# Optimization experiments

Hardware: AMD Instinct MI355X
Metric: run time of the kernel (lower is better)

Reference implementation:

```python
import jax, jax.numpy as jnp
import numpy as np

N_SAMPLES = 16_777_216  # total surviving samples across all rays
N_RAY = 65_536          # number of rays


def setup_inputs() -> dict:
    key = jax.random.key(0)
    k1, k2 = jax.random.split(key)
    alpha = jax.random.uniform(k1, (N_SAMPLES,), dtype=jnp.float32)
    # sorted ray ids -> contiguous segments, as produced by create_full_step_id + masking
    ray_id = jnp.sort(jax.random.randint(k2, (N_SAMPLES,), 0, N_RAY, dtype=jnp.int32))
    return {"alpha": alpha, "ray_id": ray_id, "N_ray": N_RAY}


def _seg_prod_op(a, b):
    # segmented-product combine: reset the running product at segment starts
    va, fa = a
    vb, fb = b
    return jnp.where(fb, vb, va * vb), fa | fb


def reference(alpha, ray_id, N_ray):
    n = alpha.shape[0]
    one_minus_alpha = 1.0 - alpha + 1e-11                      # [n]
    is_start = jnp.concatenate(
        [jnp.ones((1,), jnp.bool_), ray_id[1:] != ray_id[:-1]]
    )                                                          # [n] segment starts
    # parallel segmented cumulative product (replaces the per-sample Python loop)
    cumprod, _ = jax.lax.associative_scan(_seg_prod_op, (one_minus_alpha, is_start))
    # NOTE: faithful to the source: transmittance is a global shift of cumprod
    # (cat([1, cumprod[:-1]])), NOT reset to 1 at each ray start.
    transmittance = jnp.concatenate([jnp.ones((1,), alpha.dtype), cumprod[:-1]])
    weights = alpha * transmittance                            # [n]
    # last sample index of each ray (ids are sorted, so max index == last write)
    last_idx = jnp.zeros((N_ray,), jnp.int32).at[ray_id].max(
        jnp.arange(n, dtype=jnp.int32)
    )                                                          # [N_ray]
    alphainv_last = cumprod[last_idx]                          # [N_ray]
    return weights, alphainv_last
```

## Files before the change

### kernel.cpp

```cpp
#include <hip/hip_runtime.h>
#include <stdint.h>


#define BLOCK 256
#define PT 32
#define NV (PT / 4)
#define CHUNK (BLOCK * PT)
#define NWAVE (BLOCK / 64)

struct Pair { float v; int f; };

__device__ __forceinline__ Pair seg_combine(Pair a, Pair b) {
    Pair r;
    r.v = b.f ? b.v : (a.v * b.v);
    r.f = a.f | b.f;
    return r;
}

__global__ __launch_bounds__(BLOCK, 4)
void nerf_reduce(const float* __restrict__ alpha, const int* __restrict__ ray_id,
                 float2* __restrict__ agg, float* __restrict__ alphainv,
                 int N_ray, int n) {
    const int c = blockIdx.x, t = threadIdx.x;
    const long gstart = (long)c * CHUNK + (long)t * PT;

    {
        int gid = c * BLOCK + t;
        if (gid < N_ray) alphainv[gid] = (1.0f - alpha[0]) + 1e-11f;
    }

    Pair run; run.v = 1.0f; run.f = 0;

    if (gstart + PT <= (long)n) {
        float4 AV[NV]; int4 RV[NV];
        #pragma unroll
        for (int q = 0; q < NV; ++q) {
            AV[q] = *(const float4*)(alpha  + gstart + 4 * q);
            RV[q] = *(const int4*)  (ray_id + gstart + 4 * q);
        }
        int prev = (gstart > 0) ? ray_id[gstart - 1] : -1;

        #pragma unroll
        for (int q = 0; q < NV; ++q) {
            const float4 av = AV[q]; const int4 rv = RV[q];
            Pair e;
            e.v = (1.0f - av.x) + 1e-11f; e.f = (rv.x != prev); run = seg_combine(run, e);
            e.v = (1.0f - av.y) + 1e-11f; e.f = (rv.y != rv.x); run = seg_combine(run, e);
            e.v = (1.0f - av.z) + 1e-11f; e.f = (rv.z != rv.y); run = seg_combine(run, e);
            e.v = (1.0f - av.w) + 1e-11f; e.f = (rv.w != rv.z); run = seg_combine(run, e);
            prev = rv.w;
        }
    } else if (gstart < (long)n) {
        int prev = (gstart > 0) ? ray_id[gstart - 1] : -1;
        for (int k = 0; k < PT; ++k) {
            long g = gstart + k;
            if (g < n) {
                int r = ray_id[g];
                Pair e; e.v = (1.0f - alpha[g]) + 1e-11f; e.f = (r != prev);
                prev = r;
                run = seg_combine(run, e);
            }
        }
    }

    #pragma unroll
    for (int off = 1; off < 64; off <<= 1) {
        Pair o;
        o.v = __shfl_down(run.v, off);
        o.f = __shfl_down(run.f, off);
        run = seg_combine(run, o);
    }

    __shared__ float s_wv[NWAVE];
    __shared__ int   s_wf[NWAVE];
    const int lane = t & 63, w = t >> 6;
    if (lane == 0) { s_wv[w] = run.v; s_wf[w] = run.f; }
    __syncthreads();
    if (t == 0) {
        Pair acc; acc.v = s_wv[0]; acc.f = s_wf[0];
        #pragma unroll
        for (int ww = 1; ww < NWAVE; ++ww) {
            Pair e; e.v = s_wv[ww]; e.f = s_wf[ww];
            acc = seg_combine(acc, e);
        }
        agg[c] = make_float2(acc.v, __int_as_float(acc.f));
    }
}

__global__ void nerf_init_rest(const float* __restrict__ alpha,
                               float* __restrict__ alphainv_tail, int count) {
    int i = blockIdx.x * blockDim.x + threadIdx.x;
    if (i < count) alphainv_tail[i] = (1.0f - alpha[0]) + 1e-11f;
}

__global__ __launch_bounds__(BLOCK, 3)
void nerf_apply(const float* __restrict__ alpha, const int* __restrict__ ray_id,
                const float2* __restrict__ agg,
                float* __restrict__ weights, float* __restrict__ alphainv, int n) {
    __shared__ float s_wv[NWAVE];
    __shared__ int   s_wf[NWAVE];
    __shared__ float s_pv;
    __shared__ int   s_pf;

    const int c = blockIdx.x, t = threadIdx.x;
    const int lane = t & 63, w = t >> 6;
    const long gstart = (long)c * CHUNK + (long)t * PT;

    if (t == 0) {
        Pair pre; pre.v = 1.0f; pre.f = 0;
        for (int j = c - 1; j >= 0; --j) {
            float2 g = agg[j];
            Pair e; e.v = g.x; e.f = __float_as_int(g.y);
            pre = (j == c - 1) ? e : seg_combine(e, pre);
            if (pre.f) break;
        }
        s_pv = pre.v; s_pf = pre.f;
    }

    const bool full = (gstart + PT) <= (long)n;
    float4 AV[NV]; int4 RV[NV];
    if (full) {
        #pragma unroll
        for (int q = 0; q < NV; ++q) {
            AV[q] = *(const float4*)(alpha  + gstart + 4 * q);
            RV[q] = *(const int4*)  (ray_id + gstart + 4 * q);
        }
    } else {
        #pragma unroll
        for (int q = 0; q < NV; ++q) {
            float aa[4]; int rr[4];
            #pragma unroll
            for (int k = 0; k < 4; ++k) {
                long g = gstart + 4 * q + k;
                aa[k] = (g < n) ? alpha[g]  : 0.0f;
                rr[k] = (g < n) ? ray_id[g] : -2;
            }
            AV[q] = make_float4(aa[0], aa[1], aa[2], aa[3]);
            RV[q] = make_int4(rr[0], rr[1], rr[2], rr[3]);
        }
    }
    const int prev0 = (gstart > 0 && gstart < (long)n) ? ray_id[gstart - 1] : -1;

    Pair loc; loc.v = 1.0f; loc.f = 0;
    {
        int prev = prev0;
        #pragma unroll
        for (int q = 0; q < NV; ++q) {
            const float4 av = AV[q]; const int4 rv = RV[q];
            if (full) {
                Pair e;
                e.v = (1.0f - av.x) + 1e-11f; e.f = (rv.x != prev); loc = seg_combine(loc, e);
                e.v = (1.0f - av.y) + 1e-11f; e.f = (rv.y != rv.x); loc = seg_combine(loc, e);
                e.v = (1.0f - av.z) + 1e-11f; e.f = (rv.z != rv.y); loc = seg_combine(loc, e);
                e.v = (1.0f - av.w) + 1e-11f; e.f = (rv.w != rv.z); loc = seg_combine(loc, e);
                prev = rv.w;
            } else {
                const float aa[4] = {av.x, av.y, av.z, av.w};
                const int   rr[4] = {rv.x, rv.y, rv.z, rv.w};
                #pragma unroll
                for (int k = 0; k < 4; ++k) {
                    long g = gstart + 4 * q + k;
                    if (g < n) {
                        Pair e; e.v = (1.0f - aa[k]) + 1e-11f; e.f = (rr[k] != prev);
                        prev = rr[k];
                        loc = seg_combine(loc, e);
                    }
                }
            }
        }
    }

    Pair inc = loc;
    #pragma unroll
    for (int off = 1; off < 64; off <<= 1) {
        Pair o;
        o.v = __shfl_up(inc.v, off);
        o.f = __shfl_up(inc.f, off);
        if (lane >= off) inc = seg_combine(o, inc);
    }
    Pair lexcl;
    {
        float uv = __shfl_up(inc.v, 1);
        int   uf = __shfl_up(inc.f, 1);
        if (lane == 0) { lexcl.v = 1.0f; lexcl.f = 0; }
        else           { lexcl.v = uv;   lexcl.f = uf; }
    }
    if (lane == 63) { s_wv[w] = inc.v; s_wf[w] = inc.f; }
    __syncthreads();

    Pair base; base.v = s_pv; base.f = s_pf;
    #pragma unroll
    for (int ww = 0; ww < NWAVE; ++ww) {
        if (ww < w) {
            Pair e; e.v = s_wv[ww]; e.f = s_wf[ww];
            base = seg_combine(base, e);
        }
    }
    Pair P = seg_combine(base, lexcl);

    {
        int prevRid = prev0;
        #pragma unroll
        for (int q = 0; q < NV; ++q) {
            const float4 av = AV[q]; const int4 rv = RV[q];
            const long e0 = gstart + 4 * q;
            if (full) {
                float w0, w1, w2, w3;
                int f = (rv.x != prevRid);
                w0 = av.x * P.v;
                if (f && e0 > 0) alphainv[prevRid] = P.v;
                { Pair e; e.v = (1.0f - av.x) + 1e-11f; e.f = f; P = seg_combine(P, e); }
                if (e0 == (long)n - 1) alphainv[rv.x] = P.v;
                f = (rv.y != rv.x);
                w1 = av.y * P.v;
                if (f) alphainv[rv.x] = P.v;
                { Pair e; e.v = (1.0f - av.y) + 1e-11f; e.f = f; P = seg_combine(P, e); }
                if (e0 + 1 == (long)n - 1) alphainv[rv.y] = P.v;
                f = (rv.z != rv.y);
                w2 = av.z * P.v;
                if (f) alphainv[rv.y] = P.v;
                { Pair e; e.v = (1.0f - av.z) + 1e-11f; e.f = f; P = seg_combine(P, e); }
                if (e0 + 2 == (long)n - 1) alphainv[rv.z] = P.v;
                f = (rv.w != rv.z);
                w3 = av.w * P.v;
                if (f) alphainv[rv.z] = P.v;
                { Pair e; e.v = (1.0f - av.w) + 1e-11f; e.f = f; P = seg_combine(P, e); }
                if (e0 + 3 == (long)n - 1) alphainv[rv.w] = P.v;

                *(float4*)(weights + e0) = make_float4(w0, w1, w2, w3);
            } else {
                const float aa[4] = {av.x, av.y, av.z, av.w};
                const int   rr[4] = {rv.x, rv.y, rv.z, rv.w};
                #pragma unroll
                for (int k = 0; k < 4; ++k) {
                    long g = e0 + k;
                    if (g < n) {
                        int f = (rr[k] != prevRid);
                        float wv = aa[k] * P.v;
                        if (f && g > 0) alphainv[prevRid] = P.v;
                        { Pair e; e.v = (1.0f - aa[k]) + 1e-11f; e.f = f; P = seg_combine(P, e); }
                        if (g == (long)n - 1) alphainv[rr[k]] = P.v;
                        weights[g] = wv;
                        prevRid = rr[k];
                    }
                }
            }
            if (full) prevRid = rv.w;
        }
    }
}

extern "C" void kernel_launch(void* const* d_in, const int* in_sizes, int n_in,
                              void* d_out, int out_size, void* d_ws, size_t ws_size,
                              hipStream_t stream) {
    const float* alpha  = (const float*)d_in[0];
    const int*   ray_id = (const int*)d_in[1];
    const int n     = in_sizes[0];
    const int N_ray = out_size - n;

    float* weights  = (float*)d_out;
    float* alphainv = weights + n;
    float2* agg     = (float2*)d_ws;

    const int nchunks = (n + CHUNK - 1) / CHUNK;

    nerf_reduce<<<nchunks, BLOCK, 0, stream>>>(alpha, ray_id, agg, alphainv, N_ray, n);
    if (N_ray > nchunks * BLOCK) {
        int extra = N_ray - nchunks * BLOCK;
        nerf_init_rest<<<(extra + BLOCK - 1) / BLOCK, BLOCK, 0, stream>>>(
            alpha, alphainv + nchunks * BLOCK, extra);
    }
    nerf_apply<<<nchunks, BLOCK, 0, stream>>>(alpha, ray_id, agg, weights, alphainv, n);
}
```

Baseline: 211.0 us.

## Fuse reduce and apply passes using per-block decoupled lookback over input windows

Replaces the two-pass reduce-then-apply segmented scan with a single kernel. Each block recomputes its incoming prefix by scanning preceding 1024-element windows of the input until a segment start is found. This removes one full read of alpha and ray_id and the workspace aggregate array, at the cost of redundant window reads and extra block-level syncs per block. Weight output now uses nontemporal stores, and launch bounds are relaxed, which may reduce occupancy.

```diff
diff --git a/kernel.cpp b/kernel.cpp
--- a/kernel.cpp
+++ b/kernel.cpp
@@ -7,6 +7,9 @@
 #define NV (PT / 4)
 #define CHUNK (BLOCK * PT)
 #define NWAVE (BLOCK / 64)
+#define LOOKW 1024
+
+typedef float nat_f4 __attribute__((ext_vector_type(4)));
 
 struct Pair { float v; int f; };
 
@@ -17,105 +20,25 @@
     return r;
 }
 
-__global__ __launch_bounds__(BLOCK, 4)
-void nerf_reduce(const float* __restrict__ alpha, const int* __restrict__ ray_id,
-                 float2* __restrict__ agg, float* __restrict__ alphainv,
-                 int N_ray, int n) {
-    const int c = blockIdx.x, t = threadIdx.x;
-    const long gstart = (long)c * CHUNK + (long)t * PT;
-
-    {
-        int gid = c * BLOCK + t;
-        if (gid < N_ray) alphainv[gid] = (1.0f - alpha[0]) + 1e-11f;
-    }
-
-    Pair run; run.v = 1.0f; run.f = 0;
-
-    if (gstart + PT <= (long)n) {
-        float4 AV[NV]; int4 RV[NV];
-        #pragma unroll
-        for (int q = 0; q < NV; ++q) {
-            AV[q] = *(const float4*)(alpha  + gstart + 4 * q);
-            RV[q] = *(const int4*)  (ray_id + gstart + 4 * q);
-        }
-        int prev = (gstart > 0) ? ray_id[gstart - 1] : -1;
-
-        #pragma unroll
-        for (int q = 0; q < NV; ++q) {
-            const float4 av = AV[q]; const int4 rv = RV[q];
-            Pair e;
-            e.v = (1.0f - av.x) + 1e-11f; e.f = (rv.x != prev); run = seg_combine(run, e);
-            e.v = (1.0f - av.y) + 1e-11f; e.f = (rv.y != rv.x); run = seg_combine(run, e);
-            e.v = (1.0f - av.z) + 1e-11f; e.f = (rv.z != rv.y); run = seg_combine(run, e);
-            e.v = (1.0f - av.w) + 1e-11f; e.f = (rv.w != rv.z); run = seg_combine(run, e);
-            prev = rv.w;
-        }
-    } else if (gstart < (long)n) {
-        int prev = (gstart > 0) ? ray_id[gstart - 1] : -1;
-        for (int k = 0; k < PT; ++k) {
-            long g = gstart + k;
-            if (g < n) {
-                int r = ray_id[g];
-                Pair e; e.v = (1.0f - alpha[g]) + 1e-11f; e.f = (r != prev);
-                prev = r;
-                run = seg_combine(run, e);
-            }
-        }
-    }
-
-    #pragma unroll
-    for (int off = 1; off < 64; off <<= 1) {
-        Pair o;
-        o.v = __shfl_down(run.v, off);
-        o.f = __shfl_down(run.f, off);
-        run = seg_combine(run, o);
-    }
-
-    __shared__ float s_wv[NWAVE];
-    __shared__ int   s_wf[NWAVE];
-    const int lane = t & 63, w = t >> 6;
-    if (lane == 0) { s_wv[w] = run.v; s_wf[w] = run.f; }
-    __syncthreads();
-    if (t == 0) {
-        Pair acc; acc.v = s_wv[0]; acc.f = s_wf[0];
-        #pragma unroll
-        for (int ww = 1; ww < NWAVE; ++ww) {
-            Pair e; e.v = s_wv[ww]; e.f = s_wf[ww];
-            acc = seg_combine(acc, e);
-        }
-        agg[c] = make_float2(acc.v, __int_as_float(acc.f));
-    }
-}
-
-__global__ void nerf_init_rest(const float* __restrict__ alpha,
-                               float* __restrict__ alphainv_tail, int count) {
+__global__ void nerf_init(const float* __restrict__ alpha,
+                          float* __restrict__ alphainv, int N_ray) {
     int i = blockIdx.x * blockDim.x + threadIdx.x;
-    if (i < count) alphainv_tail[i] = (1.0f - alpha[0]) + 1e-11f;
-}
-
-__global__ __launch_bounds__(BLOCK, 3)
-void nerf_apply(const float* __restrict__ alpha, const int* __restrict__ ray_id,
-                const float2* __restrict__ agg,
+    if (i < N_ray) alphainv[i] = (1.0f - alpha[0]) + 1e-11f;
+}
+
+__global__ __launch_bounds__(BLOCK, 2)
+void nerf_fused(const float* __restrict__ alpha, const int* __restrict__ ray_id,
                 float* __restrict__ weights, float* __restrict__ alphainv, int n) {
     __shared__ float s_wv[NWAVE];
     __shared__ int   s_wf[NWAVE];
-    __shared__ float s_pv;
-    __shared__ int   s_pf;
+    __shared__ int   s_rid[BLOCK];
+    __shared__ float s_bv;
+    __shared__ int   s_bf;
 
     const int c = blockIdx.x, t = threadIdx.x;
     const int lane = t & 63, w = t >> 6;
-    const long gstart = (long)c * CHUNK + (long)t * PT;
-
-    if (t == 0) {
-        Pair pre; pre.v = 1.0f; pre.f = 0;
-        for (int j = c - 1; j >= 0; --j) {
-            float2 g = agg[j];
-            Pair e; e.v = g.x; e.f = __float_as_int(g.y);
-            pre = (j == c - 1) ? e : seg_combine(e, pre);
-            if (pre.f) break;
-        }
-        s_pv = pre.v; s_pf = pre.f;
-    }
+    const long bstart = (long)c * CHUNK;
+    const long gstart = bstart + (long)t * PT;
 
     const bool full = (gstart + PT) <= (long)n;
     float4 AV[NV]; int4 RV[NV];
@@ -140,6 +63,49 @@
         }
     }
     const int prev0 = (gstart > 0 && gstart < (long)n) ? ray_id[gstart - 1] : -1;
+
+    float P0 = 1.0f;
+    if (c > 0) {
+        long wlo = bstart - LOOKW;
+        Pair chain; chain.v = 1.0f; chain.f = 0;
+        for (;;) {
+            const long e0 = wlo + 4 * t;
+            float4 av = *(const float4*)(alpha  + e0);
+            int4   rv = *(const int4*)  (ray_id + e0);
+            s_rid[t] = rv.w;
+            __syncthreads();
+            const int prev = (t == 0) ? ((wlo > 0) ? ray_id[wlo - 1] : -1) : s_rid[t - 1];
+            Pair l;
+            l.v = (1.0f - av.x) + 1e-11f; l.f = (rv.x != prev);
+            { Pair e; e.v = (1.0f - av.y) + 1e-11f; e.f = (rv.y != rv.x); l = seg_combine(l, e); }
+            { Pair e; e.v = (1.0f - av.z) + 1e-11f; e.f = (rv.z != rv.y); l = seg_combine(l, e); }
+            { Pair e; e.v = (1.0f - av.w) + 1e-11f; e.f = (rv.w != rv.z); l = seg_combine(l, e); }
+            #pragma unroll
+            for (int off = 1; off < 64; off <<= 1) {
+                Pair o;
+                o.v = __shfl_down(l.v, off);
+                o.f = __shfl_down(l.f, off);
+                l = seg_combine(l, o);
+            }
+            if (lane == 0) { s_wv[w] = l.v; s_wf[w] = l.f; }
+            __syncthreads();
+            if (t == 0) {
+                Pair acc; acc.v = s_wv[0]; acc.f = s_wf[0];
+                #pragma unroll
+                for (int ww = 1; ww < NWAVE; ++ww) {
+                    Pair e; e.v = s_wv[ww]; e.f = s_wf[ww];
+                    acc = seg_combine(acc, e);
+                }
+                s_bv = acc.v; s_bf = acc.f;
+            }
+            __syncthreads();
+            Pair wagg; wagg.v = s_bv; wagg.f = s_bf;
+            chain = seg_combine(wagg, chain);
+            if (chain.f || wlo == 0) break;
+            wlo -= LOOKW;
+        }
+        P0 = chain.v;
+    }
 
     Pair loc; loc.v = 1.0f; loc.f = 0;
     {
@@ -188,7 +154,7 @@
     if (lane == 63) { s_wv[w] = inc.v; s_wf[w] = inc.f; }
     __syncthreads();
 
-    Pair base; base.v = s_pv; base.f = s_pf;
+    Pair base; base.v = P0; base.f = (c > 0);
     #pragma unroll
     for (int ww = 0; ww < NWAVE; ++ww) {
         if (ww < w) {
@@ -227,7 +193,9 @@
                 { Pair e; e.v = (1.0f - av.w) + 1e-11f; e.f = f; P = seg_combine(P, e); }
                 if (e0 + 3 == (long)n - 1) alphainv[rv.w] = P.v;
 
-                *(float4*)(weights + e0) = make_float4(w0, w1, w2, w3);
+                nat_f4 wv4; wv4.x = w0; wv4.y = w1; wv4.z = w2; wv4.w = w3;
+                __builtin_nontemporal_store(wv4, (nat_f4*)(weights + e0));
+                prevRid = rv.w;
             } else {
                 const float aa[4] = {av.x, av.y, av.z, av.w};
                 const int   rr[4] = {rv.x, rv.y, rv.z, rv.w};
@@ -245,7 +213,6 @@
                     }
                 }
             }
-            if (full) prevRid = rv.w;
         }
     }
 }
@@ -260,15 +227,9 @@
 
     float* weights  = (float*)d_out;
     float* alphainv = weights + n;
-    float2* agg     = (float2*)d_ws;
 
     const int nchunks = (n + CHUNK - 1) / CHUNK;
 
-    nerf_reduce<<<nchunks, BLOCK, 0, stream>>>(alpha, ray_id, agg, alphainv, N_ray, n);
-    if (N_ray > nchunks * BLOCK) {
-        int extra = N_ray - nchunks * BLOCK;
-        nerf_init_rest<<<(extra + BLOCK - 1) / BLOCK, BLOCK, 0, stream>>>(
-            alpha, alphainv + nchunks * BLOCK, extra);
-    }
-    nerf_apply<<<nchunks, BLOCK, 0, stream>>>(alpha, ray_id, agg, weights, alphainv, n);
-}
+    nerf_init<<<(N_ray + BLOCK - 1) / BLOCK, BLOCK, 0, stream>>>(alpha, alphainv, N_ray);
+    nerf_fused<<<nchunks, BLOCK, 0, stream>>>(alpha, ray_id, weights, alphainv, n);
+}
```

After: 310.8 us. 47.3% more time.
